# Optimization experiments

Hardware: AMD Instinct MI355X
Metric: run time of the kernel (lower is better)

The kernel has to match this reference:

```python
import math
import jax, jax.numpy as jnp
import numpy as np

B, C, H, W = 2, 256, 128, 128
C8 = C // 8
MAX_TOKENS = 4096
S = int(math.isqrt(MAX_TOKENS))  # 64; H,W divisible by S -> exact 2x2 mean pool


def setup_inputs() -> dict:
    key = jax.random.key(0)
    ks = jax.random.split(key, 8)
    sc = 1.0 / math.sqrt(C)
    return {
        "x": jax.random.normal(ks[0], (B, C, H, W), dtype=jnp.float32),
        "Wq": jax.random.normal(ks[1], (C8, C), dtype=jnp.float32) * sc,
        "bq": jax.random.normal(ks[2], (C8,), dtype=jnp.float32) * 0.01,
        "Wk": jax.random.normal(ks[3], (C8, C), dtype=jnp.float32) * sc,
        "bk": jax.random.normal(ks[4], (C8,), dtype=jnp.float32) * 0.01,
        "Wv": jax.random.normal(ks[5], (C, C), dtype=jnp.float32) * sc,
        "bv": jax.random.normal(ks[6], (C,), dtype=jnp.float32) * 0.01,
        # torch inits gamma to 0; use small nonzero so the attention path is exercised
        "gamma": jax.random.normal(ks[7], (1,), dtype=jnp.float32) * 0.1,
    }


def _pool_to_s(t):
    # adaptive_avg_pool2d to (S,S); exact since H%S==0, W%S==0
    b, ch, h, w = t.shape
    return t.reshape(b, ch, S, h // S, S, w // S).mean(axis=(3, 5))


def reference(x, Wq, bq, Wk, bk, Wv, bv, gamma):
    b, c, h, w = x.shape
    # 1x1 convs as channel contractions
    q = jnp.einsum('bchw,oc->bohw', x, Wq) + bq[None, :, None, None]   # (b,c8,h,w)
    k = jnp.einsum('bchw,oc->bohw', x, Wk) + bk[None, :, None, None]   # (b,c8,h,w)
    v = jnp.einsum('bchw,oc->bohw', x, Wv) + bv[None, :, None, None]   # (b,c,h,w)

    q = q.reshape(b, C8, h * w).transpose(0, 2, 1)                      # (b, hw, c8)
    if h * w > MAX_TOKENS:
        k = _pool_to_s(k)
        v = _pool_to_s(v)
    k = k.reshape(b, C8, -1)                                            # (b, c8, s2)
    v = v.reshape(b, c, -1)                                             # (b, c, s2)

    attn = jnp.einsum('btc,bcs->bts', q, k) / math.sqrt(k.shape[1])     # (b, hw, s2)
    attn = jax.nn.softmax(attn, axis=-1)
    out = jnp.einsum('bcs,bts->bct', v, attn).reshape(b, c, h, w)
    return gamma[0] * out + x
```

## Files before the change

### kernel.cpp

```cpp
#include <hip/hip_runtime.h>

typedef unsigned short u16;
typedef unsigned int u32;
typedef unsigned long long u64;
typedef float f32x4 __attribute__((ext_vector_type(4)));
typedef __bf16 bf16x8 __attribute__((ext_vector_type(8)));

__device__ __forceinline__ u16 f2bf(float f) {
  unsigned u = __float_as_uint(f);
  unsigned r = u + 0x7fffu + ((u >> 16) & 1u);
  return (u16)(r >> 16);
}
__device__ __forceinline__ u32 cvt_pk_bf16(float lo, float hi) {
  u32 r;
  asm("v_cvt_pk_bf16_f32 %0, %1, %2" : "=v"(r) : "v"(lo), "v"(hi));
  return r;
}
__device__ __forceinline__ float exp2_hw(float x) {
  float r;
  asm("v_exp_f32 %0, %1" : "=v"(r) : "v"(x));
  return r;
}
__device__ __forceinline__ bf16x8 f32x8_to_bf16x8(float4 a, float4 b) {
  union { u32 u[4]; bf16x8 v; } t;
  t.u[0] = cvt_pk_bf16(a.x, a.y);
  t.u[1] = cvt_pk_bf16(a.z, a.w);
  t.u[2] = cvt_pk_bf16(b.x, b.y);
  t.u[3] = cvt_pk_bf16(b.z, b.w);
  return t.v;
}
__device__ __forceinline__ void gload_lds16(const void* g, u16* l) {
  __builtin_amdgcn_global_load_lds(
      (const __attribute__((address_space(1))) unsigned int*)g,
      (__attribute__((address_space(3))) unsigned int*)l, 16, 0, 0);
}

#define QSCALE 0.25513936f

__global__ __launch_bounds__(256) void proj_kernel(
    const float* __restrict__ x, const float* __restrict__ Wq, const float* __restrict__ bq,
    const float* __restrict__ Wk, const float* __restrict__ bk, const float* __restrict__ Wv,
    const float* __restrict__ bv, u16* __restrict__ Qb, u16* __restrict__ Kt,
    u16* __restrict__ Vb) {
  __shared__ __align__(16) u16 smem[24576];
  const int tid = threadIdx.x;
  const int lane = tid & 63, w = tid >> 6;
  const int l15 = lane & 15, l4 = lane >> 4;
  const int bi = blockIdx.x;
  const f32x4 zero = {0.f, 0.f, 0.f, 0.f};

  if (bi >= 256) {
    u16* xt = smem;
    u16* wq = smem + 16384;
    const int j = bi - 256;
    const int b = j >> 8, tb = j & 255;
    const float* xp = x + (size_t)b * 256 * 16384 + tb * 64;

    for (int i = tid; i < 4096; i += 256) {
      int oc = i >> 7, c0 = (i & 127) * 2;
      float2 f = *reinterpret_cast<const float2*>(Wq + oc * 256 + c0);
      u32 pk = cvt_pk_bf16(f.x * QSCALE, f.y * QSCALE);
      *reinterpret_cast<u32*>((char*)wq + oc * 512 + (((c0 >> 3) ^ (oc & 7)) * 16) +
                              (c0 & 7) * 2) = pk;
    }
#pragma unroll
    for (int rr = 0; rr < 4; ++rr) {
      int c = rr * 64 + (tid >> 2);
      int tch = (tid & 3) * 16;
      const float* src = xp + (size_t)c * 16384 + tch;
#pragma unroll
      for (int u = 0; u < 4; ++u) {
        float4 f = *reinterpret_cast<const float4*>(src + u * 4);
        int t = tch + u * 4;
        *reinterpret_cast<u16*>((char*)xt + (t + 0) * 512 + (((c >> 3) ^ ((t + 0) & 7)) * 16) + (c & 7) * 2) = f2bf(f.x);
        *reinterpret_cast<u16*>((char*)xt + (t + 1) * 512 + (((c >> 3) ^ ((t + 1) & 7)) * 16) + (c & 7) * 2) = f2bf(f.y);
        *reinterpret_cast<u16*>((char*)xt + (t + 2) * 512 + (((c >> 3) ^ ((t + 2) & 7)) * 16) + (c & 7) * 2) = f2bf(f.z);
        *reinterpret_cast<u16*>((char*)xt + (t + 3) * 512 + (((c >> 3) ^ ((t + 3) & 7)) * 16) + (c & 7) * 2) = f2bf(f.w);
      }
    }
    __syncthreads();

    f32x4 acc[2] = {zero, zero};
    const int tl = w * 16 + l15;
#pragma unroll
    for (int k = 0; k < 8; ++k) {
      bf16x8 bf = *reinterpret_cast<const bf16x8*>((char*)xt + tl * 512 +
                                                   (((k * 4 + l4) ^ (tl & 7)) * 16));
#pragma unroll
      for (int m = 0; m < 2; ++m) {
        int oc = m * 16 + l15;
        bf16x8 af = *reinterpret_cast<const bf16x8*>((char*)wq + oc * 512 +
                                                     (((k * 4 + l4) ^ (oc & 7)) * 16));
        acc[m] = __builtin_amdgcn_mfma_f32_16x16x32_bf16(af, bf, acc[m], 0, 0, 0);
      }
    }
    const int t = tb * 64 + tl;
#pragma unroll
    for (int m = 0; m < 2; ++m) {
      int oc0 = m * 16 + l4 * 4;
      u32 p0 = cvt_pk_bf16(acc[m][0] + bq[oc0] * QSCALE, acc[m][1] + bq[oc0 + 1] * QSCALE);
      u32 p1 = cvt_pk_bf16(acc[m][2] + bq[oc0 + 2] * QSCALE, acc[m][3] + bq[oc0 + 3] * QSCALE);
      u16* dst = Qb + ((size_t)b * 16384 + t) * 32 + oc0;
      *reinterpret_cast<u32*>(dst) = p0;
      *reinterpret_cast<u32*>(dst + 2) = p1;
    }
  } else {
    u16* xs = smem;
    const int b = bi >> 7, r2 = bi & 127;
    const int sy = r2 >> 1, z = r2 & 1;
    const int mb = z * 8;
    const float* xb = x + (size_t)b * 256 * 16384;

#pragma unroll
    for (int rr = 0; rr < 4; ++rr) {
      int c = rr * 64 + (tid >> 2);
      int f4base = (tid & 3) * 8;
      const float* r0 = xb + (size_t)c * 16384 + (size_t)sy * 256;
#pragma unroll
      for (int u = 0; u < 8; ++u) {
        int jj = f4base + u;
        float4 a = *reinterpret_cast<const float4*>(r0 + jj * 4);
        float4 d = *reinterpret_cast<const float4*>(r0 + 128 + jj * 4);
        float p0 = (a.x + a.y + d.x + d.y) * 0.25f;
        float p1 = (a.z + a.w + d.z + d.w) * 0.25f;
        int s0 = jj * 2;
        *reinterpret_cast<u16*>((char*)xs + (s0 + 0) * 512 + (((c >> 3) ^ ((s0 + 0) & 7)) * 16) + (c & 7) * 2) = f2bf(p0);
        *reinterpret_cast<u16*>((char*)xs + (s0 + 1) * 512 + (((c >> 3) ^ ((s0 + 1) & 7)) * 16) + (c & 7) * 2) = f2bf(p1);
      }
    }
    __syncthreads();

    f32x4 acc[10];
#pragma unroll
    for (int m = 0; m < 10; ++m) acc[m] = zero;
    const int sl = w * 16 + l15;
#pragma unroll
    for (int k = 0; k < 8; ++k) {
      bf16x8 bf = *reinterpret_cast<const bf16x8*>((char*)xs + sl * 512 +
                                                   (((k * 4 + l4) ^ (sl & 7)) * 16));
      if (z == 0) {
#pragma unroll
        for (int m = 0; m < 2; ++m) {
          const float* wr = Wk + (size_t)(m * 16 + l15) * 256 + k * 32 + l4 * 8;
          float4 fa = *reinterpret_cast<const float4*>(wr);
          float4 fb = *reinterpret_cast<const float4*>(wr + 4);
          acc[m] = __builtin_amdgcn_mfma_f32_16x16x32_bf16(f32x8_to_bf16x8(fa, fb), bf, acc[m], 0, 0, 0);
        }
      }
#pragma unroll
      for (int mm = 0; mm < 8; ++mm) {
        const float* wr = Wv + (size_t)((mb + mm) * 16 + l15) * 256 + k * 32 + l4 * 8;
        float4 fa = *reinterpret_cast<const float4*>(wr);
        float4 fb = *reinterpret_cast<const float4*>(wr + 4);
        acc[2 + mm] = __builtin_amdgcn_mfma_f32_16x16x32_bf16(f32x8_to_bf16x8(fa, fb), bf, acc[2 + mm], 0, 0, 0);
      }
    }
    if (z == 0) {
#pragma unroll
      for (int m = 0; m < 2; ++m) {
        int oc0 = m * 16 + l4 * 4;
        u32 p0 = cvt_pk_bf16(acc[m][0] + bk[oc0], acc[m][1] + bk[oc0 + 1]);
        u32 p1 = cvt_pk_bf16(acc[m][2] + bk[oc0 + 2], acc[m][3] + bk[oc0 + 3]);
        u16* dst = Kt + ((size_t)b * 4096 + sy * 64 + sl) * 32 + oc0;
        *reinterpret_cast<u32*>(dst) = p0;
        *reinterpret_cast<u32*>(dst + 2) = p1;
      }
    }
#pragma unroll
    for (int mm = 0; mm < 8; ++mm) {
#pragma unroll
      for (int r = 0; r < 4; ++r) {
        int oc = (mb + mm) * 16 + l4 * 4 + r;
        Vb[((size_t)b * 256 + oc) * 4096 + sy * 64 + sl] = f2bf(acc[2 + mm][r] + bv[oc]);
      }
    }
  }
}

__global__ __launch_bounds__(512, 4) void attn_kernel(
    const u16* __restrict__ Qb, const u16* __restrict__ Kt, const u16* __restrict__ Vb,
    const float* __restrict__ x, const float* __restrict__ gamma, float* __restrict__ out) {
  __shared__ __align__(16) u16 p_lds[2][64 * 64];
  __shared__ __align__(16) u16 v_lds[256 * 64];

  const int tid = threadIdx.x;
  const int lane = tid & 63, w = tid >> 6;
  const int l15 = lane & 15, l4 = lane >> 4, l7 = l15 & 7;
  const int raw = blockIdx.x;
  const int xcd = raw & 7, loc = raw >> 3;
  const int b = xcd >> 2;
  const int tt = (xcd & 3) * 64 + loc;
  const int t0 = tt * 64;
  const int kw = w & 3, thf = w >> 2;
  const int chq = w & 3;

  const u16* Qp = Qb + (size_t)(b * 16384 + t0) * 32;
  const u16* Kp = Kt + (size_t)b * 4096 * 32;
  const char* Kpc = (const char*)Kp;
  const char* Vpc = (const char*)(Vb + (size_t)b * 256 * 4096);

  bf16x8 qfr[2];
#pragma unroll
  for (int mt = 0; mt < 2; ++mt)
    qfr[mt] = *reinterpret_cast<const bf16x8*>(Qp + (size_t)(thf * 32 + mt * 16 + l15) * 32 + l4 * 8);

  const int key = kw * 16 + l15;
  const int pw_chunk = kw * 2 + (l4 >> 1), pw_off = (l4 & 1) * 8;

  char* pA0 = (char*)p_lds + (thf * 32 + l15) * 128 + ((l4 ^ l7) * 16);
  char* pA1 = (char*)p_lds + (thf * 32 + l15) * 128 + (((4 ^ l4) ^ l7) * 16);
  char* pW = (char*)p_lds + (thf * 32 + l15) * 128 + ((pw_chunk ^ l7) * 16) + pw_off;
  char* pV0 = (char*)v_lds + (chq * 64 + l15) * 128 + ((l4 ^ l7) * 16);
  char* pV1 = (char*)v_lds + (chq * 64 + l15) * 128 + (((4 ^ l4) ^ l7) * 16);

  const int sch = lane >> 3;
  const int skc = (lane & 7) ^ sch;
  const u32 vstg0 = (u32)(w * 32 + sch) * 8192 + (u32)skc * 16;
  u32 vstg = vstg0 + 128;
  u32 vok = 2 * 4096 + (u32)key * 64 + l4 * 16;

  f32x4 acc[2][4] = {};
  float lsum[2] = {};
  const f32x4 zero = {0.f, 0.f, 0.f, 0.f};

#pragma unroll
  for (int i = 0; i < 4; ++i)
    gload_lds16(Vpc + vstg0 + i * 65536, (u16*)v_lds + (w * 4 + i) * 512);
  {
    bf16x8 k0 = *reinterpret_cast<const bf16x8*>(Kpc + (size_t)key * 64 + l4 * 16);
#pragma unroll
    for (int mt = 0; mt < 2; ++mt) {
      f32x4 s = __builtin_amdgcn_mfma_f32_16x16x32_bf16(k0, qfr[mt], zero, 0, 0, 0);
      float p0 = exp2_hw(fminf(s[0], 28.f)), p1 = exp2_hw(fminf(s[1], 28.f));
      float p2 = exp2_hw(fminf(s[2], 28.f)), p3 = exp2_hw(fminf(s[3], 28.f));
      lsum[mt] += (p0 + p1) + (p2 + p3);
      *reinterpret_cast<u64*>(pW + mt * 2048) =
          (u64)cvt_pk_bf16(p0, p1) | ((u64)cvt_pk_bf16(p2, p3) << 32);
    }
  }
  bf16x8 kfrA = *reinterpret_cast<const bf16x8*>(Kpc + (4096 + (size_t)key * 64 + l4 * 16));
  bf16x8 kfrB;
  __syncthreads();

#define ATTN_ITER(KT, CUR, KC, KN)                                                        \
  {                                                                                       \
                            \
    if ((KT) < 62) { KN = *reinterpret_cast<const bf16x8*>(Kpc + vok); vok += 4096; }     \
                                      \
    bf16x8 afr0[2], vfr0[4];                                                              \
    _Pragma("unroll") for (int mt = 0; mt < 2; ++mt)                                      \
        afr0[mt] = *reinterpret_cast<const bf16x8*>(pA0 + ((CUR)*8192 + mt * 2048));      \
    _Pragma("unroll") for (int nt = 0; nt < 4; ++nt)                                      \
        vfr0[nt] = *reinterpret_cast<const bf16x8*>(pV0 + nt * 2048);                     \
                                  \
    u64 pk0 = 0, pk1 = 0;                                                                 \
    if ((KT) < 63) {                                                                      \
      f32x4 s0 = __builtin_amdgcn_mfma_f32_16x16x32_bf16(KC, qfr[0], zero, 0, 0, 0);      \
      f32x4 s1 = __builtin_amdgcn_mfma_f32_16x16x32_bf16(KC, qfr[1], zero, 0, 0, 0);      \
      float a0 = exp2_hw(fminf(s0[0], 28.f)), a1 = exp2_hw(fminf(s0[1], 28.f));           \
      float a2 = exp2_hw(fminf(s0[2], 28.f)), a3 = exp2_hw(fminf(s0[3], 28.f));           \
      float b0 = exp2_hw(fminf(s1[0], 28.f)), b1 = exp2_hw(fminf(s1[1], 28.f));           \
      float b2 = exp2_hw(fminf(s1[2], 28.f)), b3 = exp2_hw(fminf(s1[3], 28.f));           \
      lsum[0] += (a0 + a1) + (a2 + a3);                                                   \
      lsum[1] += (b0 + b1) + (b2 + b3);                                                   \
      pk0 = (u64)cvt_pk_bf16(a0, a1) | ((u64)cvt_pk_bf16(a2, a3) << 32);                  \
      pk1 = (u64)cvt_pk_bf16(b0, b1) | ((u64)cvt_pk_bf16(b2, b3) << 32);                  \
    }                                                                                     \
                                                               \
    __builtin_amdgcn_s_setprio(1);                                                        \
    _Pragma("unroll") for (int mt = 0; mt < 2; ++mt)                                      \
      _Pragma("unroll") for (int nt = 0; nt < 4; ++nt)                                    \
        acc[mt][nt] =                                                                     \
            __builtin_amdgcn_mfma_f32_16x16x32_bf16(afr0[mt], vfr0[nt], acc[mt][nt], 0, 0, 0); \
    bf16x8 afr1[2], vfr1[4];                                                              \
    _Pragma("unroll") for (int mt = 0; mt < 2; ++mt)                                      \
        afr1[mt] = *reinterpret_cast<const bf16x8*>(pA1 + ((CUR)*8192 + mt * 2048));      \
    _Pragma("unroll") for (int nt = 0; nt < 4; ++nt)                                      \
        vfr1[nt] = *reinterpret_cast<const bf16x8*>(pV1 + nt * 2048);                     \
    _Pragma("unroll") for (int mt = 0; mt < 2; ++mt)                                      \
      _Pragma("unroll") for (int nt = 0; nt < 4; ++nt)                                    \
        acc[mt][nt] =                                                                     \
            __builtin_amdgcn_mfma_f32_16x16x32_bf16(afr1[mt], vfr1[nt], acc[mt][nt], 0, 0, 0); \
    __builtin_amdgcn_s_setprio(0);                                                        \
    __syncthreads();                    \
                    \
    if ((KT) < 63) {                                                                      \
      _Pragma("unroll") for (int i = 0; i < 4; ++i)                                       \
          gload_lds16(Vpc + vstg + i * 65536, (u16*)v_lds + (w * 4 + i) * 512);           \
      vstg += 128;                                                                        \
      *reinterpret_cast<u64*>(pW + (((CUR) ^ 1) * 8192)) = pk0;                           \
      *reinterpret_cast<u64*>(pW + (((CUR) ^ 1) * 8192 + 2048)) = pk1;                    \
    }                                                                                     \
    __syncthreads();                              \
  }

  for (int it = 0; it < 32; ++it) {
    ATTN_ITER(2 * it, 0, kfrA, kfrB)
    ATTN_ITER(2 * it + 1, 1, kfrB, kfrA)
  }
#undef ATTN_ITER

  float* lred = (float*)v_lds;
#pragma unroll
  for (int mt = 0; mt < 2; ++mt) {
    lsum[mt] += __shfl_xor(lsum[mt], 16, 64);
    lsum[mt] += __shfl_xor(lsum[mt], 32, 64);
  }
  if (l4 == 0) {
#pragma unroll
    for (int mt = 0; mt < 2; ++mt) lred[kw * 64 + thf * 32 + mt * 16 + l15] = lsum[mt];
  }
  __syncthreads();

  const float g = gamma[0];
  float linv[8];
#pragma unroll
  for (int mt = 0; mt < 2; ++mt)
#pragma unroll
    for (int r = 0; r < 4; ++r) {
      int tok = thf * 32 + mt * 16 + l4 * 4 + r;
      linv[mt * 4 + r] =
          1.0f / (lred[tok] + lred[64 + tok] + lred[128 + tok] + lred[192 + tok]);
    }
#pragma unroll
  for (int mt = 0; mt < 2; ++mt) {
#pragma unroll
    for (int nt = 0; nt < 4; ++nt) {
      int ch = chq * 64 + nt * 16 + l15;
      size_t idx = ((size_t)(b * 256 + ch)) * 16384 + t0 + thf * 32 + mt * 16 + l4 * 4;
      float4 xr = *reinterpret_cast<const float4*>(x + idx);
      float4 o;
      o.x = g * acc[mt][nt][0] * linv[mt * 4 + 0] + xr.x;
      o.y = g * acc[mt][nt][1] * linv[mt * 4 + 1] + xr.y;
      o.z = g * acc[mt][nt][2] * linv[mt * 4 + 2] + xr.z;
      o.w = g * acc[mt][nt][3] * linv[mt * 4 + 3] + xr.w;
      *reinterpret_cast<float4*>(out + idx) = o;
    }
  }
}

extern "C" void kernel_launch(void* const* d_in, const int* in_sizes, int n_in,
                              void* d_out, int out_size, void* d_ws, size_t ws_size,
                              hipStream_t stream) {
  const float* x = (const float*)d_in[0];
  const float* Wq = (const float*)d_in[1];
  const float* bq = (const float*)d_in[2];
  const float* Wk = (const float*)d_in[3];
  const float* bk = (const float*)d_in[4];
  const float* Wv = (const float*)d_in[5];
  const float* bv = (const float*)d_in[6];
  const float* gamma = (const float*)d_in[7];
  float* out = (float*)d_out;

  char* ws = (char*)d_ws;
  u16* Qb = (u16*)ws;
  u16* Kt = (u16*)(ws + (2u << 20));
  u16* Vb = (u16*)(ws + (2u << 20) + (512u << 10));

  proj_kernel<<<dim3(768), 256, 0, stream>>>(x, Wq, bq, Wk, bk, Wv, bv, Qb, Kt, Vb);
  attn_kernel<<<dim3(512), 512, 0, stream>>>(Qb, Kt, Vb, x, gamma, out);
}
```

Before: 133.5 us.

## Keep softmax probabilities in registers via permlane swaps and double-buffer V in LDS

Restructures the attention kernel so each wave owns 16 tokens and half the channels. Each wave computes scores for all 64 keys of a tile itself, which removes the shared P buffer in LDS. The probability fragments are rearranged into MFMA A-operand layout in registers using v_permlane32/16_swap, and V tiles are double-buffered in LDS so each iteration needs one barrier instead of two. This also drops the cross-wave LDS reduction of row sums in favour of shuffles. The cost is that each wave now recomputes QK for its own tokens with more K loads per wave, and the larger V buffer raises LDS use and register pressure, which may reduce occupancy.

```diff
diff --git a/kernel.cpp b/kernel.cpp
--- a/kernel.cpp
+++ b/kernel.cpp
@@ -180,8 +180,7 @@
 __global__ __launch_bounds__(512, 4) void attn_kernel(
     const u16* __restrict__ Qb, const u16* __restrict__ Kt, const u16* __restrict__ Vb,
     const float* __restrict__ x, const float* __restrict__ gamma, float* __restrict__ out) {
-  __shared__ __align__(16) u16 p_lds[2][64 * 64];
-  __shared__ __align__(16) u16 v_lds[256 * 64];
+  __shared__ __align__(16) u16 v_lds[2][256 * 64];
 
   const int tid = threadIdx.x;
   const int lane = tid & 63, w = tid >> 6;
@@ -191,107 +190,88 @@
   const int b = xcd >> 2;
   const int tt = (xcd & 3) * 64 + loc;
   const int t0 = tt * 64;
-  const int kw = w & 3, thf = w >> 2;
-  const int chq = w & 3;
+  const int tg = w >> 1, chh = w & 1;
 
   const u16* Qp = Qb + (size_t)(b * 16384 + t0) * 32;
-  const u16* Kp = Kt + (size_t)b * 4096 * 32;
-  const char* Kpc = (const char*)Kp;
+  const char* Kpc = (const char*)(Kt + (size_t)b * 4096 * 32);
   const char* Vpc = (const char*)(Vb + (size_t)b * 256 * 4096);
 
-  bf16x8 qfr[2];
-#pragma unroll
-  for (int mt = 0; mt < 2; ++mt)
-    qfr[mt] = *reinterpret_cast<const bf16x8*>(Qp + (size_t)(thf * 32 + mt * 16 + l15) * 32 + l4 * 8);
-
-  const int key = kw * 16 + l15;
-  const int pw_chunk = kw * 2 + (l4 >> 1), pw_off = (l4 & 1) * 8;
-
-  char* pA0 = (char*)p_lds + (thf * 32 + l15) * 128 + ((l4 ^ l7) * 16);
-  char* pA1 = (char*)p_lds + (thf * 32 + l15) * 128 + (((4 ^ l4) ^ l7) * 16);
-  char* pW = (char*)p_lds + (thf * 32 + l15) * 128 + ((pw_chunk ^ l7) * 16) + pw_off;
-  char* pV0 = (char*)v_lds + (chq * 64 + l15) * 128 + ((l4 ^ l7) * 16);
-  char* pV1 = (char*)v_lds + (chq * 64 + l15) * 128 + (((4 ^ l4) ^ l7) * 16);
+  const bf16x8 qfr =
+      *reinterpret_cast<const bf16x8*>(Qp + (size_t)(tg * 16 + l15) * 32 + l4 * 8);
+
+  const char* pV0 = (char*)v_lds + (chh * 128 + l15) * 128 + ((l4 ^ l7) * 16);
+  const char* pV1 = (char*)v_lds + (chh * 128 + l15) * 128 + (((4 ^ l4) ^ l7) * 16);
 
   const int sch = lane >> 3;
   const int skc = (lane & 7) ^ sch;
   const u32 vstg0 = (u32)(w * 32 + sch) * 8192 + (u32)skc * 16;
   u32 vstg = vstg0 + 128;
-  u32 vok = 2 * 4096 + (u32)key * 64 + l4 * 16;
-
-  f32x4 acc[2][4] = {};
-  float lsum[2] = {};
+  u32 vok = 4096 + (u32)l15 * 64 + (u32)l4 * 16;
+
+  f32x4 acc[8] = {};
+  float lsum = 0.f;
   const f32x4 zero = {0.f, 0.f, 0.f, 0.f};
 
 #pragma unroll
   for (int i = 0; i < 4; ++i)
     gload_lds16(Vpc + vstg0 + i * 65536, (u16*)v_lds + (w * 4 + i) * 512);
-  {
-    bf16x8 k0 = *reinterpret_cast<const bf16x8*>(Kpc + (size_t)key * 64 + l4 * 16);
-#pragma unroll
-    for (int mt = 0; mt < 2; ++mt) {
-      f32x4 s = __builtin_amdgcn_mfma_f32_16x16x32_bf16(k0, qfr[mt], zero, 0, 0, 0);
-      float p0 = exp2_hw(fminf(s[0], 28.f)), p1 = exp2_hw(fminf(s[1], 28.f));
-      float p2 = exp2_hw(fminf(s[2], 28.f)), p3 = exp2_hw(fminf(s[3], 28.f));
-      lsum[mt] += (p0 + p1) + (p2 + p3);
-      *reinterpret_cast<u64*>(pW + mt * 2048) =
-          (u64)cvt_pk_bf16(p0, p1) | ((u64)cvt_pk_bf16(p2, p3) << 32);
-    }
-  }
-  bf16x8 kfrA = *reinterpret_cast<const bf16x8*>(Kpc + (4096 + (size_t)key * 64 + l4 * 16));
-  bf16x8 kfrB;
+  bf16x8 kfrA[4], kfrB[4];
+#pragma unroll
+  for (int ka = 0; ka < 4; ++ka)
+    kfrA[ka] = *reinterpret_cast<const bf16x8*>(Kpc + (ka * 1024 + l15 * 64 + l4 * 16));
   __syncthreads();
 
-#define ATTN_ITER(KT, CUR, KC, KN)                                                        \
-  {                                                                                       \
-                            \
-    if ((KT) < 62) { KN = *reinterpret_cast<const bf16x8*>(Kpc + vok); vok += 4096; }     \
-                                      \
-    bf16x8 afr0[2], vfr0[4];                                                              \
-    _Pragma("unroll") for (int mt = 0; mt < 2; ++mt)                                      \
-        afr0[mt] = *reinterpret_cast<const bf16x8*>(pA0 + ((CUR)*8192 + mt * 2048));      \
-    _Pragma("unroll") for (int nt = 0; nt < 4; ++nt)                                      \
-        vfr0[nt] = *reinterpret_cast<const bf16x8*>(pV0 + nt * 2048);                     \
-                                  \
-    u64 pk0 = 0, pk1 = 0;                                                                 \
-    if ((KT) < 63) {                                                                      \
-      f32x4 s0 = __builtin_amdgcn_mfma_f32_16x16x32_bf16(KC, qfr[0], zero, 0, 0, 0);      \
-      f32x4 s1 = __builtin_amdgcn_mfma_f32_16x16x32_bf16(KC, qfr[1], zero, 0, 0, 0);      \
-      float a0 = exp2_hw(fminf(s0[0], 28.f)), a1 = exp2_hw(fminf(s0[1], 28.f));           \
-      float a2 = exp2_hw(fminf(s0[2], 28.f)), a3 = exp2_hw(fminf(s0[3], 28.f));           \
-      float b0 = exp2_hw(fminf(s1[0], 28.f)), b1 = exp2_hw(fminf(s1[1], 28.f));           \
-      float b2 = exp2_hw(fminf(s1[2], 28.f)), b3 = exp2_hw(fminf(s1[3], 28.f));           \
-      lsum[0] += (a0 + a1) + (a2 + a3);                                                   \
-      lsum[1] += (b0 + b1) + (b2 + b3);                                                   \
-      pk0 = (u64)cvt_pk_bf16(a0, a1) | ((u64)cvt_pk_bf16(a2, a3) << 32);                  \
-      pk1 = (u64)cvt_pk_bf16(b0, b1) | ((u64)cvt_pk_bf16(b2, b3) << 32);                  \
-    }                                                                                     \
-                                                               \
-    __builtin_amdgcn_s_setprio(1);                                                        \
-    _Pragma("unroll") for (int mt = 0; mt < 2; ++mt)                                      \
-      _Pragma("unroll") for (int nt = 0; nt < 4; ++nt)                                    \
-        acc[mt][nt] =                                                                     \
-            __builtin_amdgcn_mfma_f32_16x16x32_bf16(afr0[mt], vfr0[nt], acc[mt][nt], 0, 0, 0); \
-    bf16x8 afr1[2], vfr1[4];                                                              \
-    _Pragma("unroll") for (int mt = 0; mt < 2; ++mt)                                      \
-        afr1[mt] = *reinterpret_cast<const bf16x8*>(pA1 + ((CUR)*8192 + mt * 2048));      \
-    _Pragma("unroll") for (int nt = 0; nt < 4; ++nt)                                      \
-        vfr1[nt] = *reinterpret_cast<const bf16x8*>(pV1 + nt * 2048);                     \
-    _Pragma("unroll") for (int mt = 0; mt < 2; ++mt)                                      \
-      _Pragma("unroll") for (int nt = 0; nt < 4; ++nt)                                    \
-        acc[mt][nt] =                                                                     \
-            __builtin_amdgcn_mfma_f32_16x16x32_bf16(afr1[mt], vfr1[nt], acc[mt][nt], 0, 0, 0); \
-    __builtin_amdgcn_s_setprio(0);                                                        \
-    __syncthreads();                    \
-                    \
-    if ((KT) < 63) {                                                                      \
-      _Pragma("unroll") for (int i = 0; i < 4; ++i)                                       \
-          gload_lds16(Vpc + vstg + i * 65536, (u16*)v_lds + (w * 4 + i) * 512);           \
-      vstg += 128;                                                                        \
-      *reinterpret_cast<u64*>(pW + (((CUR) ^ 1) * 8192)) = pk0;                           \
-      *reinterpret_cast<u64*>(pW + (((CUR) ^ 1) * 8192 + 2048)) = pk1;                    \
-    }                                                                                     \
-    __syncthreads();                              \
+#define ATTN_ITER(KT, CUR, KC, KN)                                                         \
+  {                                                                                        \
+                          \
+    if ((KT) < 63) {                                                                       \
+      _Pragma("unroll") for (int i = 0; i < 4; ++i)                                        \
+          gload_lds16(Vpc + vstg + i * 65536,                                              \
+                      (u16*)v_lds + (((CUR) ^ 1) * 16384) + (w * 4 + i) * 512);            \
+      vstg += 128;                                                                         \
+    }                                                                                      \
+                         \
+    f32x4 sfr[4];                                                                          \
+    _Pragma("unroll") for (int ka = 0; ka < 4; ++ka)                                       \
+        sfr[ka] = __builtin_amdgcn_mfma_f32_16x16x32_bf16(KC[ka], qfr, zero, 0, 0, 0);     \
+    if ((KT) < 63) {                                   \
+      _Pragma("unroll") for (int ka = 0; ka < 4; ++ka)                                     \
+          KN[ka] = *reinterpret_cast<const bf16x8*>(Kpc + vok + ka * 1024);                \
+      vok += 4096;                                                                         \
+    }                                                                                      \
+                                       \
+    u32 pk[4][2];                                                                          \
+    _Pragma("unroll") for (int ka = 0; ka < 4; ++ka) {                                     \
+      float p0 = exp2_hw(fminf(sfr[ka][0], 28.f)), p1 = exp2_hw(fminf(sfr[ka][1], 28.f));  \
+      float p2 = exp2_hw(fminf(sfr[ka][2], 28.f)), p3 = exp2_hw(fminf(sfr[ka][3], 28.f));  \
+      lsum += (p0 + p1) + (p2 + p3);                                                       \
+      pk[ka][0] = cvt_pk_bf16(p0, p1);                                                     \
+      pk[ka][1] = cvt_pk_bf16(p2, p3);                                                     \
+    }                                                                                      \
+                           \
+    __builtin_amdgcn_s_setprio(1);                                                         \
+    _Pragma("unroll") for (int ks = 0; ks < 2; ++ks) {                                     \
+      union { u32 u[4]; bf16x8 v; } t;                                                     \
+      _Pragma("unroll") for (int i = 0; i < 2; ++i) {                                      \
+        u32 X = pk[2 * ks][i], Y = pk[2 * ks + 1][i];                                      \
+        asm("v_permlane32_swap_b32 %0, %1" : "+v"(X), "+v"(Y));                            \
+        asm("v_permlane16_swap_b32 %0, %1" : "+v"(X), "+v"(Y));                            \
+        t.u[i] = X;                                                                        \
+        t.u[2 + i] = Y;                                                                    \
+      }                                                                                    \
+      bf16x8 afr = t.v;                                                                    \
+      _Pragma("unroll") for (int h = 0; h < 2; ++h) {                                      \
+        bf16x8 vfr[4];                                                                     \
+        _Pragma("unroll") for (int n = 0; n < 4; ++n)                                      \
+            vfr[n] = *reinterpret_cast<const bf16x8*>((ks ? pV1 : pV0) + (CUR)*32768 +     \
+                                                      (h * 4 + n) * 2048);                 \
+        _Pragma("unroll") for (int n = 0; n < 4; ++n)                                      \
+            acc[h * 4 + n] = __builtin_amdgcn_mfma_f32_16x16x32_bf16(afr, vfr[n],          \
+                                                                     acc[h * 4 + n], 0, 0, 0); \
+      }                                                                                    \
+    }                                                                                      \
+    __builtin_amdgcn_s_setprio(0);                                                         \
+    __syncthreads();                           \
   }
 
   for (int it = 0; it < 32; ++it) {
@@ -300,42 +280,24 @@
   }
 #undef ATTN_ITER
 
-  float* lred = (float*)v_lds;
-#pragma unroll
-  for (int mt = 0; mt < 2; ++mt) {
-    lsum[mt] += __shfl_xor(lsum[mt], 16, 64);
-    lsum[mt] += __shfl_xor(lsum[mt], 32, 64);
-  }
-  if (l4 == 0) {
-#pragma unroll
-    for (int mt = 0; mt < 2; ++mt) lred[kw * 64 + thf * 32 + mt * 16 + l15] = lsum[mt];
-  }
-  __syncthreads();
-
+  lsum += __shfl_xor(lsum, 16, 64);
+  lsum += __shfl_xor(lsum, 32, 64);
   const float g = gamma[0];
-  float linv[8];
-#pragma unroll
-  for (int mt = 0; mt < 2; ++mt)
-#pragma unroll
-    for (int r = 0; r < 4; ++r) {
-      int tok = thf * 32 + mt * 16 + l4 * 4 + r;
-      linv[mt * 4 + r] =
-          1.0f / (lred[tok] + lred[64 + tok] + lred[128 + tok] + lred[192 + tok]);
-    }
-#pragma unroll
-  for (int mt = 0; mt < 2; ++mt) {
-#pragma unroll
-    for (int nt = 0; nt < 4; ++nt) {
-      int ch = chq * 64 + nt * 16 + l15;
-      size_t idx = ((size_t)(b * 256 + ch)) * 16384 + t0 + thf * 32 + mt * 16 + l4 * 4;
-      float4 xr = *reinterpret_cast<const float4*>(x + idx);
-      float4 o;
-      o.x = g * acc[mt][nt][0] * linv[mt * 4 + 0] + xr.x;
-      o.y = g * acc[mt][nt][1] * linv[mt * 4 + 1] + xr.y;
-      o.z = g * acc[mt][nt][2] * linv[mt * 4 + 2] + xr.z;
-      o.w = g * acc[mt][nt][3] * linv[mt * 4 + 3] + xr.w;
-      *reinterpret_cast<float4*>(out + idx) = o;
-    }
+  float linv[4];
+#pragma unroll
+  for (int r = 0; r < 4; ++r) linv[r] = 1.0f / __shfl(lsum, l4 * 4 + r, 64);
+
+#pragma unroll
+  for (int nt = 0; nt < 8; ++nt) {
+    int ch = chh * 128 + nt * 16 + l15;
+    size_t idx = ((size_t)(b * 256 + ch)) * 16384 + t0 + tg * 16 + l4 * 4;
+    float4 xr = *reinterpret_cast<const float4*>(x + idx);
+    float4 o;
+    o.x = g * acc[nt][0] * linv[0] + xr.x;
+    o.y = g * acc[nt][1] * linv[1] + xr.y;
+    o.z = g * acc[nt][2] * linv[2] + xr.z;
+    o.w = g * acc[nt][3] * linv[3] + xr.w;
+    *reinterpret_cast<float4*>(out + idx) = o;
   }
 }
 
```

After: 154.1 us. 1.15x slower.

## Use 4-wave attention blocks with double-buffered V tiles and one barrier per step

Applied to the files above, without the earlier changes.

Halves the attention block to 4 waves, each covering all 64 query rows and a 64-channel slice, with four query m-tiles per wave. V tiles are double-buffered in LDS, so the next tile's async load is issued at the start of each step and the second barrier per step goes away. P for the next key tile is computed and written straight into the alternate P buffer. Per-wave register use (acc 4x4) and LDS (about 80KB per block) grow, which cuts occupancy to roughly 2 blocks per CU.

```diff
diff --git a/kernel.cpp b/kernel.cpp
--- a/kernel.cpp
+++ b/kernel.cpp
@@ -177,11 +177,11 @@
   }
 }
 
-__global__ __launch_bounds__(512, 4) void attn_kernel(
+__global__ __launch_bounds__(256, 2) void attn_kernel(
     const u16* __restrict__ Qb, const u16* __restrict__ Kt, const u16* __restrict__ Vb,
     const float* __restrict__ x, const float* __restrict__ gamma, float* __restrict__ out) {
   __shared__ __align__(16) u16 p_lds[2][64 * 64];
-  __shared__ __align__(16) u16 v_lds[256 * 64];
+  __shared__ __align__(16) u16 v_lds[2][256 * 64];
 
   const int tid = threadIdx.x;
   const int lane = tid & 63, w = tid >> 6;
@@ -191,45 +191,42 @@
   const int b = xcd >> 2;
   const int tt = (xcd & 3) * 64 + loc;
   const int t0 = tt * 64;
-  const int kw = w & 3, thf = w >> 2;
-  const int chq = w & 3;
 
   const u16* Qp = Qb + (size_t)(b * 16384 + t0) * 32;
-  const u16* Kp = Kt + (size_t)b * 4096 * 32;
-  const char* Kpc = (const char*)Kp;
+  const char* Kpc = (const char*)(Kt + (size_t)b * 4096 * 32);
   const char* Vpc = (const char*)(Vb + (size_t)b * 256 * 4096);
 
-  bf16x8 qfr[2];
-#pragma unroll
-  for (int mt = 0; mt < 2; ++mt)
-    qfr[mt] = *reinterpret_cast<const bf16x8*>(Qp + (size_t)(thf * 32 + mt * 16 + l15) * 32 + l4 * 8);
-
-  const int key = kw * 16 + l15;
-  const int pw_chunk = kw * 2 + (l4 >> 1), pw_off = (l4 & 1) * 8;
-
-  char* pA0 = (char*)p_lds + (thf * 32 + l15) * 128 + ((l4 ^ l7) * 16);
-  char* pA1 = (char*)p_lds + (thf * 32 + l15) * 128 + (((4 ^ l4) ^ l7) * 16);
-  char* pW = (char*)p_lds + (thf * 32 + l15) * 128 + ((pw_chunk ^ l7) * 16) + pw_off;
-  char* pV0 = (char*)v_lds + (chq * 64 + l15) * 128 + ((l4 ^ l7) * 16);
-  char* pV1 = (char*)v_lds + (chq * 64 + l15) * 128 + (((4 ^ l4) ^ l7) * 16);
+  bf16x8 qfr[4];
+#pragma unroll
+  for (int mt = 0; mt < 4; ++mt)
+    qfr[mt] = *reinterpret_cast<const bf16x8*>(Qp + (size_t)(mt * 16 + l15) * 32 + l4 * 8);
+
+  const int key = w * 16 + l15;
+  const int pw_chunk = w * 2 + (l4 >> 1), pw_off = (l4 & 1) * 8;
+
+  char* pA0 = (char*)p_lds + l15 * 128 + ((l4 ^ l7) * 16);
+  char* pA1 = (char*)p_lds + l15 * 128 + (((4 ^ l4) ^ l7) * 16);
+  char* pW = (char*)p_lds + l15 * 128 + ((pw_chunk ^ l7) * 16) + pw_off;
+  char* pV0 = (char*)v_lds + (w * 64 + l15) * 128 + ((l4 ^ l7) * 16);
+  char* pV1 = (char*)v_lds + (w * 64 + l15) * 128 + (((4 ^ l4) ^ l7) * 16);
 
   const int sch = lane >> 3;
   const int skc = (lane & 7) ^ sch;
-  const u32 vstg0 = (u32)(w * 32 + sch) * 8192 + (u32)skc * 16;
+  const u32 vstg0 = (u32)(w * 64 + sch) * 8192 + (u32)skc * 16;
   u32 vstg = vstg0 + 128;
-  u32 vok = 2 * 4096 + (u32)key * 64 + l4 * 16;
-
-  f32x4 acc[2][4] = {};
-  float lsum[2] = {};
+  u32 vok = 2 * 4096 + (u32)key * 64 + (u32)l4 * 16;
+
+  f32x4 acc[4][4] = {};
+  float lsum[4] = {};
   const f32x4 zero = {0.f, 0.f, 0.f, 0.f};
 
 #pragma unroll
-  for (int i = 0; i < 4; ++i)
-    gload_lds16(Vpc + vstg0 + i * 65536, (u16*)v_lds + (w * 4 + i) * 512);
+  for (int i = 0; i < 8; ++i)
+    gload_lds16(Vpc + vstg0 + i * 65536, (u16*)v_lds + (w * 8 + i) * 512);
   {
-    bf16x8 k0 = *reinterpret_cast<const bf16x8*>(Kpc + (size_t)key * 64 + l4 * 16);
-#pragma unroll
-    for (int mt = 0; mt < 2; ++mt) {
+    bf16x8 k0 = *reinterpret_cast<const bf16x8*>(Kpc + ((size_t)key * 64 + l4 * 16));
+#pragma unroll
+    for (int mt = 0; mt < 4; ++mt) {
       f32x4 s = __builtin_amdgcn_mfma_f32_16x16x32_bf16(k0, qfr[mt], zero, 0, 0, 0);
       float p0 = exp2_hw(fminf(s[0], 28.f)), p1 = exp2_hw(fminf(s[1], 28.f));
       float p2 = exp2_hw(fminf(s[2], 28.f)), p3 = exp2_hw(fminf(s[3], 28.f));
@@ -244,54 +241,48 @@
 
 #define ATTN_ITER(KT, CUR, KC, KN)                                                        \
   {                                                                                       \
-                            \
-    if ((KT) < 62) { KN = *reinterpret_cast<const bf16x8*>(Kpc + vok); vok += 4096; }     \
-                                      \
-    bf16x8 afr0[2], vfr0[4];                                                              \
-    _Pragma("unroll") for (int mt = 0; mt < 2; ++mt)                                      \
+                    \
+    if ((KT) < 63) {                                                                      \
+      _Pragma("unroll") for (int i = 0; i < 8; ++i)                                       \
+          gload_lds16(Vpc + vstg + i * 65536,                                             \
+                      (u16*)v_lds + (((CUR) ^ 1) * 16384) + (w * 8 + i) * 512);           \
+      vstg += 128;                                                                        \
+    }                                                                                     \
+                              \
+    bf16x8 afr0[4], vfr0[4];                                                              \
+    _Pragma("unroll") for (int mt = 0; mt < 4; ++mt)                                      \
         afr0[mt] = *reinterpret_cast<const bf16x8*>(pA0 + ((CUR)*8192 + mt * 2048));      \
     _Pragma("unroll") for (int nt = 0; nt < 4; ++nt)                                      \
-        vfr0[nt] = *reinterpret_cast<const bf16x8*>(pV0 + nt * 2048);                     \
-                                  \
-    u64 pk0 = 0, pk1 = 0;                                                                 \
+        vfr0[nt] = *reinterpret_cast<const bf16x8*>(pV0 + ((CUR)*32768 + nt * 2048));     \
+                    \
     if ((KT) < 63) {                                                                      \
-      f32x4 s0 = __builtin_amdgcn_mfma_f32_16x16x32_bf16(KC, qfr[0], zero, 0, 0, 0);      \
-      f32x4 s1 = __builtin_amdgcn_mfma_f32_16x16x32_bf16(KC, qfr[1], zero, 0, 0, 0);      \
-      float a0 = exp2_hw(fminf(s0[0], 28.f)), a1 = exp2_hw(fminf(s0[1], 28.f));           \
-      float a2 = exp2_hw(fminf(s0[2], 28.f)), a3 = exp2_hw(fminf(s0[3], 28.f));           \
-      float b0 = exp2_hw(fminf(s1[0], 28.f)), b1 = exp2_hw(fminf(s1[1], 28.f));           \
-      float b2 = exp2_hw(fminf(s1[2], 28.f)), b3 = exp2_hw(fminf(s1[3], 28.f));           \
-      lsum[0] += (a0 + a1) + (a2 + a3);                                                   \
-      lsum[1] += (b0 + b1) + (b2 + b3);                                                   \
-      pk0 = (u64)cvt_pk_bf16(a0, a1) | ((u64)cvt_pk_bf16(a2, a3) << 32);                  \
-      pk1 = (u64)cvt_pk_bf16(b0, b1) | ((u64)cvt_pk_bf16(b2, b3) << 32);                  \
+      _Pragma("unroll") for (int mt = 0; mt < 4; ++mt) {                                  \
+        f32x4 s = __builtin_amdgcn_mfma_f32_16x16x32_bf16(KC, qfr[mt], zero, 0, 0, 0);    \
+        float p0 = exp2_hw(fminf(s[0], 28.f)), p1 = exp2_hw(fminf(s[1], 28.f));           \
+        float p2 = exp2_hw(fminf(s[2], 28.f)), p3 = exp2_hw(fminf(s[3], 28.f));           \
+        lsum[mt] += (p0 + p1) + (p2 + p3);                                                \
+        *reinterpret_cast<u64*>(pW + (((CUR) ^ 1) * 8192 + mt * 2048)) =                  \
+            (u64)cvt_pk_bf16(p0, p1) | ((u64)cvt_pk_bf16(p2, p3) << 32);                  \
+      }                                                                                   \
+      if ((KT) < 62) { KN = *reinterpret_cast<const bf16x8*>(Kpc + vok); vok += 4096; }   \
     }                                                                                     \
-                                                               \
+                                                  \
     __builtin_amdgcn_s_setprio(1);                                                        \
-    _Pragma("unroll") for (int mt = 0; mt < 2; ++mt)                                      \
+    _Pragma("unroll") for (int mt = 0; mt < 4; ++mt)                                      \
       _Pragma("unroll") for (int nt = 0; nt < 4; ++nt)                                    \
         acc[mt][nt] =                                                                     \
             __builtin_amdgcn_mfma_f32_16x16x32_bf16(afr0[mt], vfr0[nt], acc[mt][nt], 0, 0, 0); \
-    bf16x8 afr1[2], vfr1[4];                                                              \
-    _Pragma("unroll") for (int mt = 0; mt < 2; ++mt)                                      \
+    bf16x8 afr1[4], vfr1[4];                                                              \
+    _Pragma("unroll") for (int mt = 0; mt < 4; ++mt)                                      \
         afr1[mt] = *reinterpret_cast<const bf16x8*>(pA1 + ((CUR)*8192 + mt * 2048));      \
     _Pragma("unroll") for (int nt = 0; nt < 4; ++nt)                                      \
-        vfr1[nt] = *reinterpret_cast<const bf16x8*>(pV1 + nt * 2048);                     \
-    _Pragma("unroll") for (int mt = 0; mt < 2; ++mt)                                      \
+        vfr1[nt] = *reinterpret_cast<const bf16x8*>(pV1 + ((CUR)*32768 + nt * 2048));     \
+    _Pragma("unroll") for (int mt = 0; mt < 4; ++mt)                                      \
       _Pragma("unroll") for (int nt = 0; nt < 4; ++nt)                                    \
         acc[mt][nt] =                                                                     \
             __builtin_amdgcn_mfma_f32_16x16x32_bf16(afr1[mt], vfr1[nt], acc[mt][nt], 0, 0, 0); \
     __builtin_amdgcn_s_setprio(0);                                                        \
-    __syncthreads();                    \
-                    \
-    if ((KT) < 63) {                                                                      \
-      _Pragma("unroll") for (int i = 0; i < 4; ++i)                                       \
-          gload_lds16(Vpc + vstg + i * 65536, (u16*)v_lds + (w * 4 + i) * 512);           \
-      vstg += 128;                                                                        \
-      *reinterpret_cast<u64*>(pW + (((CUR) ^ 1) * 8192)) = pk0;                           \
-      *reinterpret_cast<u64*>(pW + (((CUR) ^ 1) * 8192 + 2048)) = pk1;                    \
-    }                                                                                     \
-    __syncthreads();                              \
+    __syncthreads();                                                                      \
   }
 
   for (int it = 0; it < 32; ++it) {
@@ -302,32 +293,32 @@
 
   float* lred = (float*)v_lds;
 #pragma unroll
-  for (int mt = 0; mt < 2; ++mt) {
+  for (int mt = 0; mt < 4; ++mt) {
     lsum[mt] += __shfl_xor(lsum[mt], 16, 64);
     lsum[mt] += __shfl_xor(lsum[mt], 32, 64);
   }
   if (l4 == 0) {
 #pragma unroll
-    for (int mt = 0; mt < 2; ++mt) lred[kw * 64 + thf * 32 + mt * 16 + l15] = lsum[mt];
+    for (int mt = 0; mt < 4; ++mt) lred[w * 64 + mt * 16 + l15] = lsum[mt];
   }
   __syncthreads();
 
   const float g = gamma[0];
-  float linv[8];
-#pragma unroll
-  for (int mt = 0; mt < 2; ++mt)
+  float linv[16];
+#pragma unroll
+  for (int mt = 0; mt < 4; ++mt)
 #pragma unroll
     for (int r = 0; r < 4; ++r) {
-      int tok = thf * 32 + mt * 16 + l4 * 4 + r;
+      int tok = mt * 16 + l4 * 4 + r;
       linv[mt * 4 + r] =
           1.0f / (lred[tok] + lred[64 + tok] + lred[128 + tok] + lred[192 + tok]);
     }
 #pragma unroll
-  for (int mt = 0; mt < 2; ++mt) {
+  for (int mt = 0; mt < 4; ++mt) {
 #pragma unroll
     for (int nt = 0; nt < 4; ++nt) {
-      int ch = chq * 64 + nt * 16 + l15;
-      size_t idx = ((size_t)(b * 256 + ch)) * 16384 + t0 + thf * 32 + mt * 16 + l4 * 4;
+      int ch = w * 64 + nt * 16 + l15;
+      size_t idx = ((size_t)(b * 256 + ch)) * 16384 + t0 + mt * 16 + l4 * 4;
       float4 xr = *reinterpret_cast<const float4*>(x + idx);
       float4 o;
       o.x = g * acc[mt][nt][0] * linv[mt * 4 + 0] + xr.x;
@@ -358,5 +349,5 @@
   u16* Vb = (u16*)(ws + (2u << 20) + (512u << 10));
 
   proj_kernel<<<dim3(768), 256, 0, stream>>>(x, Wq, bq, Wk, bk, Wv, bv, Qb, Kt, Vb);
-  attn_kernel<<<dim3(512), 512, 0, stream>>>(Qb, Kt, Vb, x, gamma, out);
-}
+  attn_kernel<<<dim3(512), 256, 0, stream>>>(Qb, Kt, Vb, x, gamma, out);
+}
```

After: 126.6 us. 5.1% less time.
